# Kernel tuning notes

Measured on AMD Instinct MI355X. Metric: run time of the kernel, lower is better.

## Reference

```python
import jax, jax.numpy as jnp
import numpy as np
import math

B, L, D, H = 4, 2048, 1024, 16
HD = D // H
EPS = 1e-5


def setup_inputs() -> dict:
    key = jax.random.key(0)
    ks = jax.random.split(key, 6)
    s = 1.0 / math.sqrt(D)
    return {
        "x": jax.random.normal(ks[0], (B, L, D), dtype=jnp.float32),
        "Wq": jax.random.normal(ks[1], (D, D), dtype=jnp.float32) * s,
        "bq": jnp.zeros((D,), jnp.float32),
        "Wk": jax.random.normal(ks[2], (D, D), dtype=jnp.float32) * s,
        "bk": jnp.zeros((D,), jnp.float32),
        "Wv": jax.random.normal(ks[3], (D, D), dtype=jnp.float32) * s,
        "bv": jnp.zeros((D,), jnp.float32),
        "Wo": jax.random.normal(ks[4], (D, D), dtype=jnp.float32) * s,
        "bo": jnp.zeros((D,), jnp.float32),
        "gamma": jnp.ones((D,), jnp.float32),
        "beta": jnp.zeros((D,), jnp.float32),
    }


def reference(x, Wq, bq, Wk, bk, Wv, bv, Wo, bo, gamma, beta):
    # projections -> [B, H, L, HD]
    def split_heads(t):
        return t.reshape(B, L, H, HD).transpose(0, 2, 1, 3)

    q = split_heads(x @ Wq + bq)
    k = split_heads(x @ Wk + bk)
    v = split_heads(x @ Wv + bv)

    scores = jnp.einsum("bhqd,bhkd->bhqk", q, k) / math.sqrt(HD)
    attn = jax.nn.softmax(scores, axis=-1)  # dropout p=0.0 -> identity
    out = jnp.einsum("bhqk,bhkd->bhqd", attn, v)
    out = out.transpose(0, 2, 1, 3).reshape(B, L, D)
    out = out @ Wo + bo

    # residual + LayerNorm
    y = x + out
    mu = jnp.mean(y, axis=-1, keepdims=True)
    var = jnp.mean(jnp.square(y - mu), axis=-1, keepdims=True)
    return (y - mu) * jax.lax.rsqrt(var + EPS) * gamma + beta
```

## Files before the change

kernel.cpp:

```cpp
#include <hip/hip_runtime.h>

typedef unsigned short u16;
typedef short v8s __attribute__((ext_vector_type(8)));
typedef float v4f __attribute__((ext_vector_type(4)));
typedef unsigned int v4u __attribute__((ext_vector_type(4)));

#define BB 4
#define LL 2048
#define DD 1024
#define NH 16
#define HD 64
#define QSCALE 0.18033688011112042f
#define PAD 72

__device__ __forceinline__ float bf2f(u16 u) {
  union { unsigned int i; float f; } v; v.i = ((unsigned int)u) << 16; return v.f;
}
__device__ __forceinline__ u16 f2bf(float f) {
  union { float f; unsigned int i; } v; v.f = f;
  unsigned int u = v.i;
  return (u16)((u + 0x7fffu + ((u >> 16) & 1u)) >> 16);
}
__device__ __forceinline__ void gl_lds16(const u16* g, u16* l) {
  __builtin_amdgcn_global_load_lds(
      (const __attribute__((address_space(1))) void*)g,
      (__attribute__((address_space(3))) void*)l, 16, 0, 0);
}
__device__ __forceinline__ unsigned cvtpk_bf16(float lo, float hi) {
  unsigned r;
  asm("v_cvt_pk_bf16_f32 %0, %1, %2" : "=v"(r) : "v"(lo), "v"(hi));
  return r;
}
__device__ __forceinline__ void pl32swap(unsigned& a, unsigned& b) {
  asm("v_permlane32_swap_b32 %0, %1" : "+v"(a), "+v"(b));
}
__device__ __forceinline__ void pl16swap(unsigned& a, unsigned& b) {
  asm("v_permlane16_swap_b32 %0, %1" : "+v"(a), "+v"(b));
}

__global__ __launch_bounds__(256) void fill_val(float* __restrict__ out, float v, int n) {
  int i = blockIdx.x * 256 + threadIdx.x;
  if (i < n) out[i] = v;
}

__global__ __launch_bounds__(256) void cast_x(
    const float* __restrict__ x, u16* __restrict__ Xb) {
  int i = (blockIdx.x * 256 + threadIdx.x) * 8;
  float4 a = *(const float4*)(x + i);
  float4 b = *(const float4*)(x + i + 4);
  v8s v;
  v[0] = (short)f2bf(a.x); v[1] = (short)f2bf(a.y);
  v[2] = (short)f2bf(a.z); v[3] = (short)f2bf(a.w);
  v[4] = (short)f2bf(b.x); v[5] = (short)f2bf(b.y);
  v[6] = (short)f2bf(b.z); v[7] = (short)f2bf(b.w);
  *(v8s*)(Xb + i) = v;
}

__global__ __launch_bounds__(256) void transpose_w(
    const float* __restrict__ Wq, const float* __restrict__ Wk,
    const float* __restrict__ Wv, const float* __restrict__ Wo,
    u16* __restrict__ WT) {
  __shared__ u16 tile[64][72];
  int z = blockIdx.z;
  const float* src = (z == 0) ? Wq : (z == 1) ? Wk : (z == 2) ? Wv : Wo;
  u16* dst = WT + (size_t)z * DD * DD;
  int n0 = blockIdx.x * 64, k0 = blockIdx.y * 64;
  int tid = threadIdx.x;
#pragma unroll
  for (int i = 0; i < 2; ++i) {
    int cid = i * 256 + tid;
    int r = cid >> 3, c = (cid & 7) * 8;
    const float* sp = src + (size_t)(k0 + r) * DD + n0 + c;
    float4 a = *(const float4*)sp;
    float4 b = *(const float4*)(sp + 4);
    tile[r][c + 0] = f2bf(a.x); tile[r][c + 1] = f2bf(a.y);
    tile[r][c + 2] = f2bf(a.z); tile[r][c + 3] = f2bf(a.w);
    tile[r][c + 4] = f2bf(b.x); tile[r][c + 5] = f2bf(b.y);
    tile[r][c + 6] = f2bf(b.z); tile[r][c + 7] = f2bf(b.w);
  }
  __syncthreads();
#pragma unroll
  for (int i = 0; i < 2; ++i) {
    int cid = i * 256 + tid;
    int r = cid >> 3, c = (cid & 7) * 8;
    v8s v;
#pragma unroll
    for (int j = 0; j < 8; ++j) v[j] = (short)tile[c + j][r];
    *(v8s*)(dst + (size_t)(n0 + r) * DD + k0 + c) = v;
  }
}

__global__ __launch_bounds__(256) void gemm128(
    const u16* __restrict__ Xb, const u16* __restrict__ CTX,
    const u16* __restrict__ WT,
    const float* __restrict__ bq, const float* __restrict__ bk,
    const float* __restrict__ bv, const float* __restrict__ bo,
    u16* __restrict__ Qb, u16* __restrict__ Kb, u16* __restrict__ Vtb,
    u16* __restrict__ projb, int nbase) {
  __shared__ __align__(16) u16 LDSU[4 * 64 * PAD];
  u16* As = LDSU;
  u16* Bs = LDSU + 128 * 64;

  int tid = threadIdx.x;
  int wave = tid >> 6, lane = tid & 63, quad = lane >> 4, l15 = lane & 15;
  int wr = wave >> 1, wc = wave & 1;

  int nxg = gridDim.x;
  int orig = blockIdx.y * nxg + blockIdx.x;
  int cpx = (nxg << 6) >> 3;
  int id = (orig & 7) * cpx + (orig >> 3);
  int bx = id % nxg + nbase;
  int m0 = (id / nxg) * 128;

  int mode = bx >> 3;
  int n0g = bx * 128;
  const float* bias = (mode == 0) ? bq : (mode == 1) ? bk : (mode == 2) ? bv : bo;

  const u16* Ab = ((mode == 3) ? CTX : Xb) + (size_t)m0 * DD;
  const u16* Bb = WT + (size_t)n0g * DD;
  int lrow = lane >> 3, lcol = (lane & 7) * 8;

  v4f acc[4][4] = {};

  for (int kt = 0; kt < DD / 64; ++kt) {
    int k0 = kt * 64;
    __syncthreads();
#pragma unroll
    for (int j = 0; j < 4; ++j) {
      int seg = wave * 4 + j;
      gl_lds16(Ab + (size_t)(seg * 8 + lrow) * DD + k0 + lcol, &As[seg * 512]);
      gl_lds16(Bb + (size_t)(seg * 8 + lrow) * DD + k0 + lcol, &Bs[seg * 512]);
    }
    __syncthreads();

#pragma unroll
    for (int cc = 0; cc < 2; ++cc) {
      v8s a[4], b[4];
#pragma unroll
      for (int i = 0; i < 4; ++i)
        a[i] = *(const v8s*)&As[(wr * 64 + i * 16 + l15) * 64 + cc * 32 + quad * 8];
#pragma unroll
      for (int j = 0; j < 4; ++j)
        b[j] = *(const v8s*)&Bs[(wc * 64 + j * 16 + l15) * 64 + cc * 32 + quad * 8];
#pragma unroll
      for (int i = 0; i < 4; ++i)
#pragma unroll
        for (int j = 0; j < 4; ++j)
          acc[i][j] = __builtin_amdgcn_mfma_f32_16x16x32_bf16(a[i], b[j], acc[i][j], 0, 0, 0);
    }
  }

  __syncthreads();
  u16* ct = LDSU + wave * (64 * PAD);
  int rn = lane >> 3, rk = lane & 7;

  if (mode == 2) {
#pragma unroll
    for (int j = 0; j < 4; ++j) {
      int np = j * 16 + l15;
      float bias_v = bias[(n0g + wc * 64 + np) & (DD - 1)];
#pragma unroll
      for (int i = 0; i < 4; ++i) {
        ushort4 p;
        p.x = f2bf(acc[i][j][0] + bias_v);
        p.y = f2bf(acc[i][j][1] + bias_v);
        p.z = f2bf(acc[i][j][2] + bias_v);
        p.w = f2bf(acc[i][j][3] + bias_v);
        *(ushort4*)&ct[np * PAD + i * 16 + quad * 4] = p;
      }
    }
    int b = (m0 + wr * 64) >> 11;
    int lb = (m0 + wr * 64) & (LL - 1);
#pragma unroll
    for (int g = 0; g < 8; ++g) {
      int np = g * 8 + rn;
      int n = (n0g + wc * 64 + np) & (DD - 1);
      int h = n >> 6, d = n & 63;
      v8s v = *(const v8s*)&ct[np * PAD + rk * 8];
      *(v8s*)&Vtb[((size_t)(b * NH + h) * HD + d) * LL + lb + rk * 8] = v;
    }
  } else {
#pragma unroll
    for (int j = 0; j < 4; ++j) {
      int np = j * 16 + l15;
      float bias_v = bias[(n0g + wc * 64 + np) & (DD - 1)];
#pragma unroll
      for (int i = 0; i < 4; ++i)
#pragma unroll
        for (int r = 0; r < 4; ++r) {
          float v = acc[i][j][r] + bias_v;
          if (mode == 0) v *= QSCALE;
          ct[(i * 16 + quad * 4 + r) * PAD + np] = f2bf(v);
        }
    }
    int nb = (n0g + wc * 64) & (DD - 1);
    int h = nb >> 6;
    u16* qk = (mode == 0) ? Qb : Kb;
#pragma unroll
    for (int g = 0; g < 8; ++g) {
      int mp = g * 8 + rn;
      int m_g = m0 + wr * 64 + mp;
      v8s v = *(const v8s*)&ct[mp * PAD + rk * 8];
      if (mode == 3) {
        *(v8s*)&projb[(size_t)m_g * DD + nb + rk * 8] = v;
      } else {
        int b = m_g >> 11, l = m_g & (LL - 1);
        *(v8s*)&qk[((size_t)(b * NH + h) * LL + l) * HD + rk * 8] = v;
      }
    }
  }
}

__global__ __launch_bounds__(256, 4) void attn(
    const u16* __restrict__ Qb, const u16* __restrict__ Kb,
    const u16* __restrict__ Vtb, u16* __restrict__ ctx) {
  __shared__ __align__(16) u16 Ks[64 * PAD];
  __shared__ __align__(16) u16 Vs[64 * PAD];

  int tid = threadIdx.x;
  int wave = tid >> 6, lane = tid & 63, quad = lane >> 4, l15 = lane & 15;

  int orig = blockIdx.y * gridDim.x + blockIdx.x;
  int cpx = (gridDim.x * gridDim.y) >> 3;
  int id = (orig & 7) * cpx + (orig >> 3);
  int q0 = (id & (gridDim.x - 1)) * 128;
  int bh = id / gridDim.x;

  v8s aq[2][2];
#pragma unroll
  for (int s2 = 0; s2 < 2; ++s2) {
    const u16* Qp = Qb + ((size_t)bh * LL + q0 + s2 * 64 + wave * 16 + l15) * HD;
    aq[s2][0] = *(const v8s*)(Qp + quad * 8);
    aq[s2][1] = *(const v8s*)(Qp + 32 + quad * 8);
  }

  v4f o[2][4] = {};
  float ls2[2] = {0.f, 0.f};

  const u16* Kbase = Kb + (size_t)bh * LL * HD;
  const u16* Vbase = Vtb + (size_t)bh * HD * LL;

  for (int kt = 0; kt < LL / 64; ++kt) {
    int k0 = kt * 64;
    __syncthreads();
#pragma unroll
    for (int i = 0; i < 2; ++i) {
      int cid = i * 256 + tid;
      int r = cid >> 3, c = (cid & 7) * 8;
      *(v8s*)&Ks[r * PAD + c] = *(const v8s*)(Kbase + (size_t)(k0 + r) * HD + c);
      *(v8s*)&Vs[r * PAD + c] = *(const v8s*)(Vbase + (size_t)r * LL + k0 + c);
    }
    __syncthreads();

    v8s ak[4][2];
#pragma unroll
    for (int t = 0; t < 4; ++t) {
      ak[t][0] = *(const v8s*)&Ks[(t * 16 + l15) * PAD + quad * 8];
      ak[t][1] = *(const v8s*)&Ks[(t * 16 + l15) * PAD + 32 + quad * 8];
    }

    v8s ap[2][2];
#pragma unroll
    for (int s2 = 0; s2 < 2; ++s2) {
      v4f s[4];
#pragma unroll
      for (int t = 0; t < 4; ++t) {
        v4f z = {};
        z = __builtin_amdgcn_mfma_f32_16x16x32_bf16(ak[t][0], aq[s2][0], z, 0, 0, 0);
        s[t] = __builtin_amdgcn_mfma_f32_16x16x32_bf16(ak[t][1], aq[s2][1], z, 0, 0, 0);
      }
      unsigned W[4][2];
      float psum = 0.f;
#pragma unroll
      for (int t = 0; t < 4; ++t) {
        float p0 = __builtin_amdgcn_exp2f(s[t][0] - 64.f);
        float p1 = __builtin_amdgcn_exp2f(s[t][1] - 64.f);
        float p2 = __builtin_amdgcn_exp2f(s[t][2] - 64.f);
        float p3 = __builtin_amdgcn_exp2f(s[t][3] - 64.f);
        psum += (p0 + p1) + (p2 + p3);
        W[t][0] = cvtpk_bf16(p0, p1);
        W[t][1] = cvtpk_bf16(p2, p3);
      }
      ls2[s2] += psum;
      union { v4u u; v8s s8; } c0, c1;
#pragma unroll
      for (int j = 0; j < 2; ++j) {
        unsigned a = W[0][j], b = W[1][j];
        pl32swap(a, b); pl16swap(a, b);
        c0.u[j] = a; c0.u[2 + j] = b;
        unsigned a2 = W[2][j], b2 = W[3][j];
        pl32swap(a2, b2); pl16swap(a2, b2);
        c1.u[j] = a2; c1.u[2 + j] = b2;
      }
      ap[s2][0] = c0.s8; ap[s2][1] = c1.s8;
    }

#pragma unroll
    for (int t = 0; t < 4; ++t) {
      v8s vb0 = *(const v8s*)&Vs[(t * 16 + l15) * PAD + quad * 8];
      v8s vb1 = *(const v8s*)&Vs[(t * 16 + l15) * PAD + 32 + quad * 8];
#pragma unroll
      for (int s2 = 0; s2 < 2; ++s2) {
        o[s2][t] = __builtin_amdgcn_mfma_f32_16x16x32_bf16(ap[s2][0], vb0, o[s2][t], 0, 0, 0);
        o[s2][t] = __builtin_amdgcn_mfma_f32_16x16x32_bf16(ap[s2][1], vb1, o[s2][t], 0, 0, 0);
      }
    }
  }

  int b = bh >> 4, h = bh & 15;
#pragma unroll
  for (int s2 = 0; s2 < 2; ++s2) {
    float tot = ls2[s2];
    tot += __shfl_xor(tot, 16);
    tot += __shfl_xor(tot, 32);
    float recip = 1.f / tot;
#pragma unroll
    for (int r = 0; r < 4; ++r) {
      float inv = __shfl(recip, quad * 4 + r);
      int l = q0 + s2 * 64 + wave * 16 + quad * 4 + r;
#pragma unroll
      for (int t = 0; t < 4; ++t)
        ctx[((size_t)(b * LL + l)) * DD + h * HD + t * 16 + l15] =
            f2bf(o[s2][t][r] * inv);
    }
  }
}

__global__ __launch_bounds__(256) void resid_ln(
    const float* __restrict__ x, const u16* __restrict__ projb,
    const float* __restrict__ gamma, const float* __restrict__ beta,
    float* __restrict__ out) {
  int row = blockIdx.x, tid = threadIdx.x;
  int base = tid * 4;
  float4 xv = *(const float4*)(x + (size_t)row * DD + base);
  ushort4 pv = *(const ushort4*)(projb + (size_t)row * DD + base);
  float y0 = xv.x + bf2f(pv.x), y1 = xv.y + bf2f(pv.y);
  float y2 = xv.z + bf2f(pv.z), y3 = xv.w + bf2f(pv.w);

  float s = y0 + y1 + y2 + y3;
  s += __shfl_xor(s, 1);  s += __shfl_xor(s, 2);  s += __shfl_xor(s, 4);
  s += __shfl_xor(s, 8);  s += __shfl_xor(s, 16); s += __shfl_xor(s, 32);
  __shared__ float red[8];
  int wv = tid >> 6, ln = tid & 63;
  if (ln == 0) red[wv] = s;
  __syncthreads();
  float mu = (red[0] + red[1] + red[2] + red[3]) * (1.f / DD);

  float d0 = y0 - mu, d1 = y1 - mu, d2 = y2 - mu, d3 = y3 - mu;
  float vv = d0 * d0 + d1 * d1 + d2 * d2 + d3 * d3;
  vv += __shfl_xor(vv, 1);  vv += __shfl_xor(vv, 2);  vv += __shfl_xor(vv, 4);
  vv += __shfl_xor(vv, 8);  vv += __shfl_xor(vv, 16); vv += __shfl_xor(vv, 32);
  if (ln == 0) red[4 + wv] = vv;
  __syncthreads();
  float var = (red[4] + red[5] + red[6] + red[7]) * (1.f / DD);
  float rstd = rsqrtf(var + 1e-5f);

  float4 gv = *(const float4*)(gamma + base);
  float4 bv = *(const float4*)(beta + base);
  float4 ov;
  ov.x = d0 * rstd * gv.x + bv.x;
  ov.y = d1 * rstd * gv.y + bv.y;
  ov.z = d2 * rstd * gv.z + bv.z;
  ov.w = d3 * rstd * gv.w + bv.w;
  *(float4*)(out + (size_t)row * DD + base) = ov;
}

extern "C" void kernel_launch(void* const* d_in, const int* in_sizes, int n_in,
                              void* d_out, int out_size, void* d_ws, size_t ws_size,
                              hipStream_t stream) {
  (void)ws_size;
  float* out = (float*)d_out;

  bool ok = (n_in == 11) && (out_size == BB * LL * DD);
  if (ok) {
    const int want[11] = {BB * LL * DD, DD * DD, DD, DD * DD, DD, DD * DD,
                          DD, DD * DD, DD, DD, DD};
    for (int i = 0; i < 11; ++i) ok = ok && (in_sizes[i] == want[i]);
  }
  if (!ok) {
    fill_val<<<(out_size + 255) / 256, 256, 0, stream>>>(out, 1000.0f, out_size);
    return;
  }

  const float* x     = (const float*)d_in[0];
  const float* Wq    = (const float*)d_in[1];
  const float* bq    = (const float*)d_in[2];
  const float* Wk    = (const float*)d_in[3];
  const float* bk    = (const float*)d_in[4];
  const float* Wv    = (const float*)d_in[5];
  const float* bv    = (const float*)d_in[6];
  const float* Wo    = (const float*)d_in[7];
  const float* bo    = (const float*)d_in[8];
  const float* gamma = (const float*)d_in[9];
  const float* beta  = (const float*)d_in[10];

  char* ws = (char*)d_ws;
  u16* WT   = (u16*)(ws);
  u16* Xb   = (u16*)(ws + (size_t)8 * 1024 * 1024);
  u16* Qb   = (u16*)(ws + (size_t)24 * 1024 * 1024);
  u16* Kb   = (u16*)(ws + (size_t)40 * 1024 * 1024);
  u16* Vtb  = (u16*)(ws + (size_t)56 * 1024 * 1024);
  u16* ctxO = (u16*)d_out;
  u16* projb = Xb;

  cast_x<<<4096, 256, 0, stream>>>(x, Xb);
  transpose_w<<<dim3(16, 16, 4), 256, 0, stream>>>(Wq, Wk, Wv, Wo, WT);
  gemm128<<<dim3(24, 64), 256, 0, stream>>>(Xb, ctxO, WT, bq, bk, bv, bo,
                                            Qb, Kb, Vtb, projb, 0);
  attn<<<dim3(LL / 128, BB * NH), 256, 0, stream>>>(Qb, Kb, Vtb, ctxO);
  gemm128<<<dim3(8, 64), 256, 0, stream>>>(Xb, ctxO, WT, bq, bk, bv, bo,
                                           Qb, Kb, Vtb, projb, 24);
  resid_ln<<<8192, 256, 0, stream>>>(x, projb, gamma, beta, out);
}
```

Measured before the change: 312.1 us.

## Replace 128x128 projection GEMM with pipelined 256x256 double-buffered GEMM

The projection GEMM moves from 128x128 tiles with 4 waves to 256x256 tiles with 8 waves. Shared memory is double-buffered and XOR-swizzled, and global-to-LDS loads are interleaved into four MFMA phases with explicit vmcnt waits, barriers and setprio. The aim is to raise data reuse per tile, hide load latency behind compute, and avoid LDS bank conflicts. In exchange it uses 128KB LDS per block and more accumulator registers, and launches fewer workgroups (384 and 128), which may leave CUs underutilized.

```diff
diff --git a/kernel.cpp b/kernel.cpp
--- a/kernel.cpp
+++ b/kernel.cpp
@@ -37,6 +37,10 @@
 __device__ __forceinline__ void pl16swap(unsigned& a, unsigned& b) {
   asm("v_permlane16_swap_b32 %0, %1" : "+v"(a), "+v"(b));
 }
+
+#define MFMA16(a, b, c) __builtin_amdgcn_mfma_f32_16x16x32_bf16((a), (b), (c), 0, 0, 0)
+#define VMCNT(n) asm volatile("s_waitcnt vmcnt(" #n ")" ::: "memory")
+#define SBAR() __builtin_amdgcn_s_barrier()
 
 __global__ __launch_bounds__(256) void fill_val(float* __restrict__ out, float v, int n) {
   int i = blockIdx.x * 256 + threadIdx.x;
@@ -90,119 +94,194 @@
   }
 }
 
-__global__ __launch_bounds__(256) void gemm128(
+__global__ __launch_bounds__(512, 2) void gemm256(
     const u16* __restrict__ Xb, const u16* __restrict__ CTX,
     const u16* __restrict__ WT,
     const float* __restrict__ bq, const float* __restrict__ bk,
     const float* __restrict__ bv, const float* __restrict__ bo,
     u16* __restrict__ Qb, u16* __restrict__ Kb, u16* __restrict__ Vtb,
     u16* __restrict__ projb, int nbase) {
-  __shared__ __align__(16) u16 LDSU[4 * 64 * PAD];
-  u16* As = LDSU;
-  u16* Bs = LDSU + 128 * 64;
+  __shared__ __align__(16) u16 LDSU16[65536];
 
   int tid = threadIdx.x;
   int wave = tid >> 6, lane = tid & 63, quad = lane >> 4, l15 = lane & 15;
-  int wr = wave >> 1, wc = wave & 1;
-
-  int nxg = gridDim.x;
-  int orig = blockIdx.y * nxg + blockIdx.x;
-  int cpx = (nxg << 6) >> 3;
-  int id = (orig & 7) * cpx + (orig >> 3);
-  int bx = id % nxg + nbase;
-  int m0 = (id / nxg) * 128;
-
-  int mode = bx >> 3;
-  int n0g = bx * 128;
+  int wr = wave >> 2, wc = wave & 3;
+
+  int nwg = gridDim.x * gridDim.y;
+  int orig = blockIdx.y * gridDim.x + blockIdx.x;
+  int id = (orig & 7) * (nwg >> 3) + (orig >> 3);
+  int mb = id & 31, nb = id >> 5;
+  int m0 = mb * 256;
+  int bx = nb + nbase;
+  int mode = bx >> 2;
+  int n0g = bx * 256;
   const float* bias = (mode == 0) ? bq : (mode == 1) ? bk : (mode == 2) ? bv : bo;
 
   const u16* Ab = ((mode == 3) ? CTX : Xb) + (size_t)m0 * DD;
   const u16* Bb = WT + (size_t)n0g * DD;
-  int lrow = lane >> 3, lcol = (lane & 7) * 8;
-
-  v4f acc[4][4] = {};
-
-  for (int kt = 0; kt < DD / 64; ++kt) {
-    int k0 = kt * 64;
-    __syncthreads();
-#pragma unroll
-    for (int j = 0; j < 4; ++j) {
-      int seg = wave * 4 + j;
-      gl_lds16(Ab + (size_t)(seg * 8 + lrow) * DD + k0 + lcol, &As[seg * 512]);
-      gl_lds16(Bb + (size_t)(seg * 8 + lrow) * DD + k0 + lcol, &Bs[seg * 512]);
-    }
-    __syncthreads();
-
-#pragma unroll
-    for (int cc = 0; cc < 2; ++cc) {
-      v8s a[4], b[4];
-#pragma unroll
-      for (int i = 0; i < 4; ++i)
-        a[i] = *(const v8s*)&As[(wr * 64 + i * 16 + l15) * 64 + cc * 32 + quad * 8];
-#pragma unroll
-      for (int j = 0; j < 4; ++j)
-        b[j] = *(const v8s*)&Bs[(wc * 64 + j * 16 + l15) * 64 + cc * 32 + quad * 8];
-#pragma unroll
-      for (int i = 0; i < 4; ++i)
-#pragma unroll
-        for (int j = 0; j < 4; ++j)
-          acc[i][j] = __builtin_amdgcn_mfma_f32_16x16x32_bf16(a[i], b[j], acc[i][j], 0, 0, 0);
-    }
-  }
-
-  __syncthreads();
-  u16* ct = LDSU + wave * (64 * PAD);
-  int rn = lane >> 3, rk = lane & 7;
+
+  int srow = wave * 8 + (lane >> 3);
+  int schunk = (lane & 7) ^ ((lane >> 3) & 7);
+  const u16* srcA = Ab + (size_t)srow * DD + schunk * 8;
+  const u16* srcB = Bb + (size_t)srow * DD + schunk * 8;
+
+#define ISS_A(u, kk, bs) gl_lds16(srcA + (size_t)(u) * 64 * DD + (kk), \
+                                  &LDSU16[(bs) * 32768 + (u) * 4096 + wave * 512])
+#define ISS_B(u, kk, bs) gl_lds16(srcB + (size_t)(u) * 64 * DD + (kk), \
+                                  &LDSU16[(bs) * 32768 + 16384 + (u) * 4096 + wave * 512])
+
+  int swz = l15 & 7;
+  int c0 = (quad ^ swz) * 8, c1 = ((4 + quad) ^ swz) * 8;
+  int aoff0 = (wr * 128 + l15) * 64 + c0;
+  int aoff1 = (wr * 128 + l15) * 64 + c1;
+  int boff0 = (wc * 64 + l15) * 64 + c0;
+  int boff1 = (wc * 64 + l15) * 64 + c1;
+
+  v8s aR[4][2], bR[4][2];
+  v4f acc[8][4] = {};
+
+  ISS_A(0, 0, 0); ISS_A(2, 0, 0);
+  ISS_B(0, 0, 0); ISS_B(1, 0, 0); ISS_B(2, 0, 0); ISS_B(3, 0, 0);
+  ISS_A(1, 0, 0); ISS_A(3, 0, 0);
+  VMCNT(2);
+  SBAR();
+
+#pragma unroll 1
+  for (int t = 0; t < 16; ++t) {
+    int cur = t & 1, nxt = cur ^ 1;
+    int kn = (t + 1) * 64;
+    const u16* LA = &LDSU16[cur * 32768];
+    const u16* LB = LA + 16384;
+
+#pragma unroll
+    for (int i = 0; i < 4; ++i) {
+      aR[i][0] = *(const v8s*)&LA[aoff0 + i * 1024];
+      aR[i][1] = *(const v8s*)&LA[aoff1 + i * 1024];
+    }
+#pragma unroll
+    for (int j = 0; j < 2; ++j) {
+      bR[j][0] = *(const v8s*)&LB[boff0 + j * 1024];
+      bR[j][1] = *(const v8s*)&LB[boff1 + j * 1024];
+    }
+    if (t < 15) { ISS_A(0, kn, nxt); ISS_A(2, kn, nxt); }
+    SBAR();
+    __builtin_amdgcn_s_setprio(1);
+#pragma unroll
+    for (int i = 0; i < 4; ++i)
+#pragma unroll
+      for (int j = 0; j < 2; ++j) {
+        acc[i][j] = MFMA16(aR[i][0], bR[j][0], acc[i][j]);
+        acc[i][j] = MFMA16(aR[i][1], bR[j][1], acc[i][j]);
+      }
+    __builtin_amdgcn_s_setprio(0);
+    SBAR();
+
+#pragma unroll
+    for (int j = 0; j < 2; ++j) {
+      bR[2 + j][0] = *(const v8s*)&LB[boff0 + (2 + j) * 1024];
+      bR[2 + j][1] = *(const v8s*)&LB[boff1 + (2 + j) * 1024];
+    }
+    if (t < 15) { ISS_B(0, kn, nxt); ISS_B(1, kn, nxt); }
+    SBAR();
+    __builtin_amdgcn_s_setprio(1);
+#pragma unroll
+    for (int i = 0; i < 4; ++i)
+#pragma unroll
+      for (int j = 0; j < 2; ++j) {
+        acc[i][2 + j] = MFMA16(aR[i][0], bR[2 + j][0], acc[i][2 + j]);
+        acc[i][2 + j] = MFMA16(aR[i][1], bR[2 + j][1], acc[i][2 + j]);
+      }
+    __builtin_amdgcn_s_setprio(0);
+    if (t < 15) { VMCNT(4); } else { VMCNT(0); }
+    SBAR();
+
+#pragma unroll
+    for (int i = 0; i < 4; ++i) {
+      aR[i][0] = *(const v8s*)&LA[aoff0 + (4 + i) * 1024];
+      aR[i][1] = *(const v8s*)&LA[aoff1 + (4 + i) * 1024];
+    }
+    if (t < 15) { ISS_B(2, kn, nxt); ISS_B(3, kn, nxt); }
+    SBAR();
+    __builtin_amdgcn_s_setprio(1);
+#pragma unroll
+    for (int i = 0; i < 4; ++i)
+#pragma unroll
+      for (int j = 0; j < 2; ++j) {
+        acc[4 + i][2 + j] = MFMA16(aR[i][0], bR[2 + j][0], acc[4 + i][2 + j]);
+        acc[4 + i][2 + j] = MFMA16(aR[i][1], bR[2 + j][1], acc[4 + i][2 + j]);
+      }
+    __builtin_amdgcn_s_setprio(0);
+    SBAR();
+
+    if (t < 15) { ISS_A(1, kn, nxt); ISS_A(3, kn, nxt); }
+    SBAR();
+    __builtin_amdgcn_s_setprio(1);
+#pragma unroll
+    for (int i = 0; i < 4; ++i)
+#pragma unroll
+      for (int j = 0; j < 2; ++j) {
+        acc[4 + i][j] = MFMA16(aR[i][0], bR[j][0], acc[4 + i][j]);
+        acc[4 + i][j] = MFMA16(aR[i][1], bR[j][1], acc[4 + i][j]);
+      }
+    __builtin_amdgcn_s_setprio(0);
+    if (t < 15) { VMCNT(2); }
+    SBAR();
+  }
+#undef ISS_A
+#undef ISS_B
+
+  int nbcol = (n0g + wc * 64) & (DD - 1);
+  u16* ct = &LDSU16[wave * 8192];
+  int mbase = m0 + wr * 128;
 
   if (mode == 2) {
 #pragma unroll
-    for (int j = 0; j < 4; ++j) {
-      int np = j * 16 + l15;
-      float bias_v = bias[(n0g + wc * 64 + np) & (DD - 1)];
-#pragma unroll
-      for (int i = 0; i < 4; ++i) {
+    for (int nf = 0; nf < 4; ++nf) {
+      int np = nf * 16 + l15;
+      float bias_v = bias[(nbcol + np) & (DD - 1)];
+#pragma unroll
+      for (int mf = 0; mf < 8; ++mf) {
         ushort4 p;
-        p.x = f2bf(acc[i][j][0] + bias_v);
-        p.y = f2bf(acc[i][j][1] + bias_v);
-        p.z = f2bf(acc[i][j][2] + bias_v);
-        p.w = f2bf(acc[i][j][3] + bias_v);
-        *(ushort4*)&ct[np * PAD + i * 16 + quad * 4] = p;
-      }
-    }
-    int b = (m0 + wr * 64) >> 11;
-    int lb = (m0 + wr * 64) & (LL - 1);
-#pragma unroll
-    for (int g = 0; g < 8; ++g) {
-      int np = g * 8 + rn;
-      int n = (n0g + wc * 64 + np) & (DD - 1);
+        p.x = f2bf(acc[mf][nf][0] + bias_v);
+        p.y = f2bf(acc[mf][nf][1] + bias_v);
+        p.z = f2bf(acc[mf][nf][2] + bias_v);
+        p.w = f2bf(acc[mf][nf][3] + bias_v);
+        *(ushort4*)&ct[np * 128 + mf * 16 + quad * 4] = p;
+      }
+    }
+    int b = mbase >> 11, lb = mbase & (LL - 1);
+#pragma unroll
+    for (int g = 0; g < 16; ++g) {
+      int np = g * 4 + quad;
+      int n = (nbcol + np) & (DD - 1);
       int h = n >> 6, d = n & 63;
-      v8s v = *(const v8s*)&ct[np * PAD + rk * 8];
-      *(v8s*)&Vtb[((size_t)(b * NH + h) * HD + d) * LL + lb + rk * 8] = v;
+      v8s v = *(const v8s*)&ct[np * 128 + l15 * 8];
+      *(v8s*)&Vtb[((size_t)(b * NH + h) * HD + d) * LL + lb + l15 * 8] = v;
     }
   } else {
 #pragma unroll
-    for (int j = 0; j < 4; ++j) {
-      int np = j * 16 + l15;
-      float bias_v = bias[(n0g + wc * 64 + np) & (DD - 1)];
-#pragma unroll
-      for (int i = 0; i < 4; ++i)
+    for (int nf = 0; nf < 4; ++nf) {
+      int np = nf * 16 + l15;
+      float bias_v = bias[(nbcol + np) & (DD - 1)];
+#pragma unroll
+      for (int mf = 0; mf < 8; ++mf)
 #pragma unroll
         for (int r = 0; r < 4; ++r) {
-          float v = acc[i][j][r] + bias_v;
+          float v = acc[mf][nf][r] + bias_v;
           if (mode == 0) v *= QSCALE;
-          ct[(i * 16 + quad * 4 + r) * PAD + np] = f2bf(v);
+          ct[(mf * 16 + quad * 4 + r) * 64 + np] = f2bf(v);
         }
     }
-    int nb = (n0g + wc * 64) & (DD - 1);
-    int h = nb >> 6;
+    int rn = lane >> 3, rk = lane & 7;
+    int h = nbcol >> 6;
     u16* qk = (mode == 0) ? Qb : Kb;
 #pragma unroll
-    for (int g = 0; g < 8; ++g) {
-      int mp = g * 8 + rn;
-      int m_g = m0 + wr * 64 + mp;
-      v8s v = *(const v8s*)&ct[mp * PAD + rk * 8];
+    for (int g = 0; g < 16; ++g) {
+      int row = g * 8 + rn;
+      int m_g = mbase + row;
+      v8s v = *(const v8s*)&ct[row * 64 + rk * 8];
       if (mode == 3) {
-        *(v8s*)&projb[(size_t)m_g * DD + nb + rk * 8] = v;
+        *(v8s*)&projb[(size_t)m_g * DD + nbcol + rk * 8] = v;
       } else {
         int b = m_g >> 11, l = m_g & (LL - 1);
         *(v8s*)&qk[((size_t)(b * NH + h) * LL + l) * HD + rk * 8] = v;
@@ -282,17 +361,17 @@
         W[t][1] = cvtpk_bf16(p2, p3);
       }
       ls2[s2] += psum;
-      union { v4u u; v8s s8; } c0, c1;
+      union { v4u u; v8s s8; } cc0, cc1;
 #pragma unroll
       for (int j = 0; j < 2; ++j) {
         unsigned a = W[0][j], b = W[1][j];
         pl32swap(a, b); pl16swap(a, b);
-        c0.u[j] = a; c0.u[2 + j] = b;
+        cc0.u[j] = a; cc0.u[2 + j] = b;
         unsigned a2 = W[2][j], b2 = W[3][j];
         pl32swap(a2, b2); pl16swap(a2, b2);
-        c1.u[j] = a2; c1.u[2 + j] = b2;
-      }
-      ap[s2][0] = c0.s8; ap[s2][1] = c1.s8;
+        cc1.u[j] = a2; cc1.u[2 + j] = b2;
+      }
+      ap[s2][0] = cc0.s8; ap[s2][1] = cc1.s8;
     }
 
 #pragma unroll
@@ -405,10 +484,10 @@
 
   cast_x<<<4096, 256, 0, stream>>>(x, Xb);
   transpose_w<<<dim3(16, 16, 4), 256, 0, stream>>>(Wq, Wk, Wv, Wo, WT);
-  gemm128<<<dim3(24, 64), 256, 0, stream>>>(Xb, ctxO, WT, bq, bk, bv, bo,
+  gemm256<<<dim3(12, 32), 512, 0, stream>>>(Xb, ctxO, WT, bq, bk, bv, bo,
                                             Qb, Kb, Vtb, projb, 0);
   attn<<<dim3(LL / 128, BB * NH), 256, 0, stream>>>(Qb, Kb, Vtb, ctxO);
-  gemm128<<<dim3(8, 64), 256, 0, stream>>>(Xb, ctxO, WT, bq, bk, bv, bo,
-                                           Qb, Kb, Vtb, projb, 24);
+  gemm256<<<dim3(4, 32), 512, 0, stream>>>(Xb, ctxO, WT, bq, bk, bv, bo,
+                                           Qb, Kb, Vtb, projb, 12);
   resid_ln<<<8192, 256, 0, stream>>>(x, projb, gamma, beta, out);
 }
```

Result: no change. 308.0 us (-1.3%).
